# Optimization experiments

Hardware: AMD Instinct MI355X
Metric: run time of the kernel (lower is better)

Reference implementation:

```python
import jax, jax.numpy as jnp
import numpy as np

B, T, F, H, L = 16384, 24, 7, 8, 4
DENSE = [T * H, 1024, 2048, 4]


def setup_inputs() -> dict:
    key = jax.random.key(0)
    d = {"x": jax.random.normal(jax.random.fold_in(key, 0), (B, T, F), jnp.float32)}
    k = 1
    s = 1.0 / np.sqrt(H)  # torch LSTM init bound
    for l in range(L):
        in_dim = F if l == 0 else H
        for name, shape in [("Wih", (4 * H, in_dim)), ("Whh", (4 * H, H)), ("bih", (4 * H,)), ("bhh", (4 * H,))]:
            d[f"{name}{l}"] = jax.random.uniform(jax.random.fold_in(key, k), shape, jnp.float32, -s, s)
            k += 1
    for i in range(1, len(DENSE)):
        si = 1.0 / np.sqrt(DENSE[i - 1])
        d[f"Wd{i}"] = jax.random.uniform(jax.random.fold_in(key, k), (DENSE[i], DENSE[i - 1]), jnp.float32, -si, si)
        k += 1
        d[f"bd{i}"] = jax.random.uniform(jax.random.fold_in(key, k), (DENSE[i],), jnp.float32, -si, si)
        k += 1
    return d


def _lstm_layer(xs, Wih, Whh, b):
    # xs: [T, B, in] -> ys: [T, B, H]; torch gate order i,f,g,o
    Hn = Whh.shape[1]
    h0 = jnp.zeros((xs.shape[1], Hn), xs.dtype)

    def step(carry, xt):
        h, c = carry
        z = xt @ Wih.T + h @ Whh.T + b  # [B, 4H]
        i, f, g, o = jnp.split(z, 4, axis=-1)
        c = jax.nn.sigmoid(f) * c + jax.nn.sigmoid(i) * jnp.tanh(g)
        h = jax.nn.sigmoid(o) * jnp.tanh(c)
        return (h, c), h

    (_, _), ys = jax.lax.scan(step, (h0, h0), xs)
    return ys


def _forward(x, lstm_params, dense_params):
    xs = jnp.transpose(x, (1, 0, 2))  # [T, B, F]
    for (Wih, Whh, bih, bhh) in lstm_params:
        xs = _lstm_layer(xs, Wih, Whh, bih + bhh)
    out = jnp.transpose(xs, (1, 0, 2)).reshape(x.shape[0], T * H)  # [B, 192]
    (W1, b1), (W2, b2), (W3, b3) = dense_params
    out = jax.nn.relu(out @ W1.T + b1)
    out = jax.nn.relu(out @ W2.T + b2)
    return out @ W3.T + b3  # [B, num_classes]


def reference(x, Wih0, Whh0, bih0, bhh0, Wih1, Whh1, bih1, bhh1, Wih2, Whh2, bih2, bhh2, Wih3, Whh3, bih3, bhh3, Wd1, bd1, Wd2, bd2, Wd3, bd3):
    lstm_params = [(Wih0, Whh0, bih0, bhh0), (Wih1, Whh1, bih1, bhh1), (Wih2, Whh2, bih2, bhh2), (Wih3, Whh3, bih3, bhh3)]
    dense_params = [(Wd1, bd1), (Wd2, bd2), (Wd3, bd3)]
    return _forward(x, lstm_params, dense_params)
```

## Files before the change

kernel.cpp:

```cpp
#include <hip/hip_runtime.h>
#include <hip/hip_bf16.h>

typedef __attribute__((ext_vector_type(4))) float f32x4;
typedef __attribute__((ext_vector_type(16))) float f32x16;
typedef __attribute__((ext_vector_type(2))) float f32x2;
typedef __attribute__((ext_vector_type(8))) short bf16x8;

__device__ __forceinline__ ushort f2bf(float f) {
    union { float f; uint u; } v; v.f = f;
    uint u = v.u;
    return (ushort)((u + 0x7fffu + ((u >> 16) & 1u)) >> 16);
}
__device__ __forceinline__ float sigm(float x) {
    return __builtin_amdgcn_rcpf(1.0f + __builtin_amdgcn_exp2f(x * -1.442695040888963f));
}
__device__ __forceinline__ float tanh_(float x) {
    return 2.0f * __builtin_amdgcn_rcpf(1.0f + __builtin_amdgcn_exp2f(x * -2.885390081777927f)) - 1.0f;
}

typedef const __attribute__((address_space(1))) unsigned int ga_u32;
typedef __attribute__((address_space(3))) unsigned int lds_u32;
__device__ __forceinline__ void g2l16(const void* g, void* l) {
    __builtin_amdgcn_global_load_lds((ga_u32*)(unsigned long long)g,
                                     (lds_u32*)(unsigned int)(unsigned long long)l,
                                     16, 0, 0);
}

struct LstmW {
    const float* wih[4];
    const float* whh[4];
    const float* bih[4];
    const float* bhh[4];
};

__device__ __forceinline__ void gates8p(const f32x2 w01[8], const f32x2 w23[8],
                                        const float xv8[8], f32x2& a01, f32x2& a23) {
#pragma unroll
    for (int k = 0; k < 8; ++k) {
        f32x2 xv = {xv8[k], xv8[k]};
        a01 += w01[k] * xv;
        a23 += w23[k] * xv;
    }
}
__device__ __forceinline__ void cellup(f32x2 a01, f32x2 a23, float& h, float& c) {
    c = sigm(a01.y) * c + sigm(a01.x) * tanh_(a23.x);
    h = sigm(a23.y) * tanh_(c);
}
__device__ __forceinline__ void ld8(const float* p, float v[8]) {
    float4 a = *(const float4*)p;
    float4 b = *(const float4*)(p + 4);
    v[0] = a.x; v[1] = a.y; v[2] = a.z; v[3] = a.w;
    v[4] = b.x; v[5] = b.y; v[6] = b.z; v[7] = b.w;
}

__global__ __launch_bounds__(256) void pre_kernel(const float* __restrict__ x, LstmW p,
                                                  ushort* __restrict__ Y,
                                                  const float* __restrict__ W1,
                                                  const float* __restrict__ W2,
                                                  ushort* __restrict__ W1b,
                                                  ushort* __restrict__ W2b,
                                                  const float* __restrict__ b3,
                                                  float* __restrict__ out) {
    __shared__ float xs[32 * 168];
    __shared__ float hb[32 * 200];

    const int tid = threadIdx.x;
    if (blockIdx.x >= 512) {
        const int tg = (blockIdx.x - 512) * 256 + tid;
        if (tg < 16384) {
            float4 bv = {b3[0], b3[1], b3[2], b3[3]};
            ((float4*)out)[tg] = bv;
        }
#pragma unroll
        for (int s = 0; s < 4; ++s) {
            int i = tg + s * 143360;
            const float4* src; ushort4* dst; int off;
            if (i < 49152) { src = (const float4*)W1; dst = (ushort4*)W1b; off = i; }
            else { src = (const float4*)W2; dst = (ushort4*)W2b; off = i - 49152; }
            float4 v = src[off];
            ushort4 r; r.x = f2bf(v.x); r.y = f2bf(v.y); r.z = f2bf(v.z); r.w = f2bf(v.w);
            dst[off] = r;
        }
        return;
    }

    const int e0 = blockIdx.x * 32;
    {
        const float4* s = (const float4*)(x + (size_t)e0 * 168);
        float4* d = (float4*)xs;
        for (int i = tid; i < 1344; i += 256) d[i] = s[i];
    }
    __syncthreads();

    const int el = tid >> 3, j = tid & 7;
    float* hr = hb + el * 200;
    const float* xr = xs + el * 168;

    f32x2 wx01[8], wx23[8], wh01[8], wh23[8], b01, b23;

    {
        const float* Wih = p.wih[0];
        const float* Whh = p.whh[0];
#pragma unroll
        for (int k = 0; k < 7; ++k) {
            wx01[k] = {Wih[(0 + j) * 7 + k], Wih[(8 + j) * 7 + k]};
            wx23[k] = {Wih[(16 + j) * 7 + k], Wih[(24 + j) * 7 + k]};
        }
#pragma unroll
        for (int k = 0; k < 8; ++k) {
            wh01[k] = {Whh[(0 + j) * 8 + k], Whh[(8 + j) * 8 + k]};
            wh23[k] = {Whh[(16 + j) * 8 + k], Whh[(24 + j) * 8 + k]};
        }
        b01 = {p.bih[0][j] + p.bhh[0][j], p.bih[0][8 + j] + p.bhh[0][8 + j]};
        b23 = {p.bih[0][16 + j] + p.bhh[0][16 + j], p.bih[0][24 + j] + p.bhh[0][24 + j]};

        float h = 0.f, c = 0.f;
        {
            f32x2 a01 = b01, a23 = b23;
#pragma unroll
            for (int k = 0; k < 7; ++k) {
                f32x2 xv = {xr[k], xr[k]};
                a01 += wx01[k] * xv; a23 += wx23[k] * xv;
            }
            cellup(a01, a23, h, c);
            hr[j] = h;
        }
        for (int t = 1; t < 24; ++t) {
            f32x2 a01 = b01, a23 = b23;
#pragma unroll
            for (int k = 0; k < 7; ++k) {
                f32x2 xv = {xr[t * 7 + k], xr[t * 7 + k]};
                a01 += wx01[k] * xv; a23 += wx23[k] * xv;
            }
            float hp[8]; ld8(&hr[(t - 1) * 8], hp);
            gates8p(wh01, wh23, hp, a01, a23);
            cellup(a01, a23, h, c);
            hr[t * 8 + j] = h;
        }
    }

#pragma unroll
    for (int l = 1; l < 4; ++l) {
        const float* Wih = p.wih[l];
        const float* Whh = p.whh[l];
#pragma unroll
        for (int k = 0; k < 8; ++k) {
            wx01[k] = {Wih[(0 + j) * 8 + k], Wih[(8 + j) * 8 + k]};
            wx23[k] = {Wih[(16 + j) * 8 + k], Wih[(24 + j) * 8 + k]};
            wh01[k] = {Whh[(0 + j) * 8 + k], Whh[(8 + j) * 8 + k]};
            wh23[k] = {Whh[(16 + j) * 8 + k], Whh[(24 + j) * 8 + k]};
        }
        b01 = {p.bih[l][j] + p.bhh[l][j], p.bih[l][8 + j] + p.bhh[l][8 + j]};
        b23 = {p.bih[l][16 + j] + p.bhh[l][16 + j], p.bih[l][24 + j] + p.bhh[l][24 + j]};

        float h = 0.f, c = 0.f;
        {
            float xin[8]; ld8(&hr[0], xin);
            f32x2 a01 = b01, a23 = b23;
            gates8p(wx01, wx23, xin, a01, a23);
            cellup(a01, a23, h, c);
            hr[j] = h;
            if (l == 3) Y[((size_t)(e0 + el) * 24) * 8 + j] = f2bf(h);
        }
        for (int t = 1; t < 24; ++t) {
            float xin[8]; ld8(&hr[t * 8], xin);
            float hp[8];  ld8(&hr[(t - 1) * 8], hp);
            f32x2 a01 = b01, a23 = b23;
            gates8p(wx01, wx23, xin, a01, a23);
            gates8p(wh01, wh23, hp, a01, a23);
            cellup(a01, a23, h, c);
            hr[t * 8 + j] = h;
            if (l == 3) Y[((size_t)(e0 + el) * 24 + t) * 8 + j] = f2bf(h);
        }
    }
}

template <int KDIM>
__device__ __forceinline__ void gemm_body(const ushort* __restrict__ A,
                                          const ushort* __restrict__ W,
                                          const float* __restrict__ bias,
                                          ushort* __restrict__ Hout, int N) {
    __shared__ alignas(16) ushort smem[16384];
    ushort* As = smem;
    ushort* Ws = smem + 8192;

    const int tid = threadIdx.x;
    const int m0 = blockIdx.x * 128;
    const int n0 = blockIdx.y * 128;
    const int lane = tid & 63;
    const int wv = tid >> 6;
    const int wm = (wv & 1) * 64;
    const int wn = (wv >> 1) * 64;
    const int l31 = lane & 31;
    const int kh = lane >> 5;

    const int lrow = lane >> 3;
    const int lchunk = (lane & 7) ^ lrow;
    const ushort* Ag = A + (size_t)(m0 + wv * 32 + lrow) * KDIM + lchunk * 8;
    const ushort* Wg = W + (size_t)(n0 + wv * 32 + lrow) * KDIM + lchunk * 8;
    ushort* Ald = As + wv * 2048;
    ushort* Wld = Ws + wv * 2048;

    const int r7 = l31 & 7;
    const int arow0 = (wm + l31) * 64;
    const int brow0 = (wn + l31) * 64;

    f32x16 acc[2][2];
#pragma unroll
    for (int mi = 0; mi < 2; ++mi)
#pragma unroll
        for (int ni = 0; ni < 2; ++ni)
#pragma unroll
            for (int r = 0; r < 16; ++r) acc[mi][ni][r] = 0.f;

    for (int k0 = 0; k0 < KDIM; k0 += 64) {
#pragma unroll
        for (int c = 0; c < 4; ++c)
            g2l16(Ag + (size_t)c * 8 * KDIM + k0, Ald + c * 512);
#pragma unroll
        for (int c = 0; c < 4; ++c)
            g2l16(Wg + (size_t)c * 8 * KDIM + k0, Wld + c * 512);
        __syncthreads();

#pragma unroll
        for (int ks = 0; ks < 4; ++ks) {
            const int ck = ((ks * 2 + kh) ^ r7) * 8;
            bf16x8 afr[2], bfr[2];
#pragma unroll
            for (int mi = 0; mi < 2; ++mi)
                afr[mi] = *(const bf16x8*)&As[arow0 + mi * 2048 + ck];
#pragma unroll
            for (int ni = 0; ni < 2; ++ni)
                bfr[ni] = *(const bf16x8*)&Ws[brow0 + ni * 2048 + ck];
#pragma unroll
            for (int mi = 0; mi < 2; ++mi)
#pragma unroll
                for (int ni = 0; ni < 2; ++ni)
                    acc[mi][ni] = __builtin_amdgcn_mfma_f32_32x32x16_bf16(afr[mi], bfr[ni],
                                                                         acc[mi][ni], 0, 0, 0);
        }
        __syncthreads();
    }

#pragma unroll
    for (int ni = 0; ni < 2; ++ni) {
        const int col = n0 + wn + ni * 32 + l31;
        const float b = bias[col];
#pragma unroll
        for (int mi = 0; mi < 2; ++mi)
#pragma unroll
            for (int r = 0; r < 16; ++r) {
                const int row = m0 + wm + mi * 32 + (r & 3) + 8 * (r >> 2) + 4 * kh;
                Hout[(size_t)row * N + col] = f2bf(fmaxf(acc[mi][ni][r] + b, 0.f));
            }
    }
}

__global__ __launch_bounds__(256, 4) void gemm1_kernel(const ushort* __restrict__ A,
                                                       const ushort* __restrict__ W,
                                                       const float* __restrict__ bias,
                                                       ushort* __restrict__ Hout, int N) {
    gemm_body<192>(A, W, bias, Hout, N);
}

template <int OFFB>
__device__ __forceinline__ bf16x8 dsr(unsigned a) {
    bf16x8 r;
    asm volatile("ds_read_b128 %0, %1 offset:%2"
                 : "=v"(r) : "v"(a), "i"(OFFB));
    return r;
}
template <int B>
__device__ __forceinline__ void ld_ah_asm(unsigned p0, unsigned p1, bf16x8 fr[8]) {
    fr[0] = dsr<B + 0>(p0);    fr[1] = dsr<B + 0>(p1);
    fr[2] = dsr<B + 2048>(p0); fr[3] = dsr<B + 2048>(p1);
    fr[4] = dsr<B + 4096>(p0); fr[5] = dsr<B + 4096>(p1);
    fr[6] = dsr<B + 6144>(p0); fr[7] = dsr<B + 6144>(p1);
}
template <int B>
__device__ __forceinline__ void ld_bh_asm(unsigned p0, unsigned p1, bf16x8 fr[4]) {
    fr[0] = dsr<B + 0>(p0);    fr[1] = dsr<B + 0>(p1);
    fr[2] = dsr<B + 2048>(p0); fr[3] = dsr<B + 2048>(p1);
}
template <int QA, int QB>
__device__ __forceinline__ void mma_quad(f32x4 acc[8][4], const bf16x8 afr[8],
                                         const bf16x8 bfr[4]) {
#pragma unroll
    for (int ks = 0; ks < 2; ++ks)
#pragma unroll
        for (int mi = 0; mi < 4; ++mi)
#pragma unroll
            for (int ni = 0; ni < 2; ++ni)
                acc[QA * 4 + mi][QB * 2 + ni] = __builtin_amdgcn_mfma_f32_16x16x32_bf16(
                    afr[mi * 2 + ks], bfr[ni * 2 + ks], acc[QA * 4 + mi][QB * 2 + ni],
                    0, 0, 0);
}

#define SBAR() __builtin_amdgcn_s_barrier()
#define MMA_GATE() do { SBAR(); \
    asm volatile("s_waitcnt lgkmcnt(0)"); \
    __builtin_amdgcn_sched_barrier(0); } while (0)
#define CLUSTER_END() do { __builtin_amdgcn_s_setprio(0); \
    __builtin_amdgcn_sched_barrier(0); } while (0)

__global__ __launch_bounds__(512) void gemm2_kernel(const ushort* __restrict__ A,
                                                    const ushort* __restrict__ W,
                                                    const float* __restrict__ bias,
                                                    const float* __restrict__ W3,
                                                    float* __restrict__ outf) {
    __shared__ alignas(16) ushort smem[65536];
    __shared__ alignas(16) float w3s[1040];

    const int tid = threadIdx.x;
    const int wg = ((int)blockIdx.x & 7) * 64 + ((int)blockIdx.x >> 3);
    const int m0 = (wg >> 3) << 8;
    const int n0 = (wg & 7) << 8;

    const int lane = tid & 63;
    const int wv = tid >> 6;

    const int lrow = tid >> 3;
    const int lc8 = ((tid & 7) ^ (lrow & 7)) << 3;
    const ushort* Ag = A + (size_t)(m0 + lrow) * 1024 + lc8;
    const ushort* Bg = W + (size_t)(n0 + lrow) * 1024 + lc8;
    ushort* const sA0 = smem;
    ushort* const sB0 = smem + 16384;
    ushort* const sA1 = smem + 32768;
    ushort* const sB1 = smem + 49152;
    const int srow64 = (wv << 3) * 64;

    const int l15 = lane & 15, kq = lane >> 4, r7 = l15 & 7;
    const int wM = wv >> 2, wN = wv & 3;
    const unsigned sbase = (unsigned)(unsigned long long)&smem[0];
    const unsigned pc0B = (unsigned)((kq ^ r7) << 4);
    const unsigned pc1B = pc0B ^ 64u;
    const unsigned aRowB = (unsigned)((wM * 128 + l15) * 128);
    const unsigned bRowB = (unsigned)((wN * 64 + l15) * 128);
    const unsigned aA0p0 = sbase + aRowB + pc0B;
    const unsigned aA0p1 = sbase + aRowB + pc1B;
    const unsigned aA1p0 = aA0p0 + 65536u;
    const unsigned aA1p1 = aA0p1 + 65536u;
    const unsigned bB0p0 = sbase + 32768u + bRowB + pc0B;
    const unsigned bB0p1 = sbase + 32768u + bRowB + pc1B;
    const unsigned bB1p0 = bB0p0 + 65536u;
    const unsigned bB1p1 = bB0p1 + 65536u;

    auto stA = [&](int buf, int h, int kt) {
        ushort* b = buf ? sA1 : sA0;
#pragma unroll
        for (int c = 0; c < 2; ++c)
            g2l16(Ag + (size_t)(h * 128 + c * 64) * 1024 + kt * 64,
                  b + (h * 128 + c * 64) * 64 + srow64);
    };
    auto stB = [&](int buf, int h, int kt) {
        ushort* b = buf ? sB1 : sB0;
#pragma unroll
        for (int c = 0; c < 2; ++c)
            g2l16(Bg + (size_t)(h * 128 + c * 64) * 1024 + kt * 64,
                  b + (h * 128 + c * 64) * 64 + srow64);
    };

    f32x4 acc[8][4];
#pragma unroll
    for (int i = 0; i < 8; ++i)
#pragma unroll
        for (int j = 0; j < 4; ++j)
#pragma unroll
            for (int r = 0; r < 4; ++r) acc[i][j][r] = 0.f;

#pragma unroll
    for (int i = 0; i < 2; ++i) {
        int idx = tid + i * 512;
        w3s[(idx >> 8) * 260 + (idx & 255)] = W3[(size_t)(idx >> 8) * 2048 + n0 + (idx & 255)];
    }
    float bias4[4];
#pragma unroll
    for (int ni = 0; ni < 4; ++ni) bias4[ni] = bias[n0 + wN * 64 + ni * 16 + l15];

    stA(0, 0, 0); stB(0, 0, 0); stB(0, 1, 0); stA(0, 1, 0);
    stB(1, 0, 1); stB(1, 1, 1);
    asm volatile("s_waitcnt vmcnt(0)" ::: "memory");
    SBAR();

    bf16x8 afr[8], b0r[4], b1r[4];
#pragma unroll 1
    for (int it = 0; it < 8; ++it) {
        const int k1 = 2 * it + 1, k2 = 2 * it + 2, k3 = 2 * it + 3;
        const bool nl = (it < 7);
        ld_ah_asm<0>(aA0p0, aA0p1, afr);
        ld_bh_asm<0>(bB0p0, bB0p1, b0r);
        stA(1, 0, k1);
        MMA_GATE();
        __builtin_amdgcn_s_setprio(1);
        mma_quad<0, 0>(acc, afr, b0r);
        CLUSTER_END();
        SBAR();
        ld_bh_asm<4096>(bB0p0, bB0p1, b1r);
        stA(1, 1, k1);
        MMA_GATE();
        __builtin_amdgcn_s_setprio(1);
        mma_quad<0, 1>(acc, afr, b1r);
        CLUSTER_END();
        SBAR();
        ld_ah_asm<8192>(aA0p0, aA0p1, afr);
        if (nl) stB(0, 0, k2);
        MMA_GATE();
        __builtin_amdgcn_s_setprio(1);
        mma_quad<1, 1>(acc, afr, b1r);
        CLUSTER_END();
        SBAR();
        if (nl) stB(0, 1, k2);
        MMA_GATE();
        __builtin_amdgcn_s_setprio(1);
        mma_quad<1, 0>(acc, afr, b0r);
        CLUSTER_END();
        if (nl) { asm volatile("s_waitcnt vmcnt(4)" ::: "memory"); }
        else    { asm volatile("s_waitcnt vmcnt(0)" ::: "memory"); }
        SBAR();
        ld_ah_asm<8192>(aA1p0, aA1p1, afr);
        ld_bh_asm<0>(bB1p0, bB1p1, b0r);
        if (nl) stA(0, 0, k2);
        MMA_GATE();
        __builtin_amdgcn_s_setprio(1);
        mma_quad<1, 0>(acc, afr, b0r);
        CLUSTER_END();
        SBAR();
        ld_bh_asm<4096>(bB1p0, bB1p1, b1r);
        if (nl) stA(0, 1, k2);
        MMA_GATE();
        __builtin_amdgcn_s_setprio(1);
        mma_quad<1, 1>(acc, afr, b1r);
        CLUSTER_END();
        SBAR();
        ld_ah_asm<0>(aA1p0, aA1p1, afr);
        if (nl) stB(1, 0, k3);
        MMA_GATE();
        __builtin_amdgcn_s_setprio(1);
        mma_quad<0, 1>(acc, afr, b1r);
        CLUSTER_END();
        SBAR();
        if (nl) stB(1, 1, k3);
        MMA_GATE();
        __builtin_amdgcn_s_setprio(1);
        mma_quad<0, 0>(acc, afr, b0r);
        CLUSTER_END();
        if (nl) { asm volatile("s_waitcnt vmcnt(4)" ::: "memory"); }
        SBAR();
    }

    float* Cs = (float*)smem;
    const int drow = tid >> 3;
    const int cls = (tid & 7) >> 1;
    const int hf = tid & 1;
    const float* wrow = &w3s[cls * 260 + hf * 128];
    __syncthreads();
#pragma unroll
    for (int s = 0; s < 4; ++s) {
        if (wM == (s >> 1)) {
            const int mb = (s & 1) * 4;
#pragma unroll
            for (int mi = 0; mi < 4; ++mi)
#pragma unroll
                for (int ni = 0; ni < 4; ++ni) {
                    f32x4 v = acc[mb + mi][ni];
                    const int cbase = (mi * 16 + kq * 4) * 260 + wN * 64 + ni * 16 + l15;
#pragma unroll
                    for (int r = 0; r < 4; ++r)
                        Cs[cbase + r * 260] = fmaxf(v[r] + bias4[ni], 0.f);
                }
        }
        __syncthreads();
        {
            const float* crow = &Cs[drow * 260 + hf * 128];
            float p = 0.f;
#pragma unroll
            for (int ch = 0; ch < 64; ++ch) {
                f32x2 cv = *(const f32x2*)(crow + ch * 2);
                f32x2 wv2 = *(const f32x2*)(wrow + ch * 2);
                p += cv.x * wv2.x + cv.y * wv2.y;
            }
            p += __shfl_xor(p, 1);
            if (hf == 0)
                atomicAdd(&outf[(size_t)(m0 + s * 64 + drow) * 4 + cls], p);
        }
        __syncthreads();
    }
}

extern "C" void kernel_launch(void* const* d_in, const int* in_sizes, int n_in,
                              void* d_out, int out_size, void* d_ws, size_t ws_size,
                              hipStream_t stream) {
    const float* x = (const float*)d_in[0];
    LstmW w;
    for (int l = 0; l < 4; ++l) {
        w.wih[l] = (const float*)d_in[1 + 4 * l];
        w.whh[l] = (const float*)d_in[2 + 4 * l];
        w.bih[l] = (const float*)d_in[3 + 4 * l];
        w.bhh[l] = (const float*)d_in[4 + 4 * l];
    }
    const float* Wd1 = (const float*)d_in[17];
    const float* bd1 = (const float*)d_in[18];
    const float* Wd2 = (const float*)d_in[19];
    const float* bd2 = (const float*)d_in[20];
    const float* Wd3 = (const float*)d_in[21];
    const float* bd3 = (const float*)d_in[22];
    float* out = (float*)d_out;

    ushort* Y   = (ushort*)d_ws;
    ushort* H1  = (ushort*)((char*)d_ws + 6291456);
    ushort* W1b = (ushort*)((char*)d_ws + 39845888);
    ushort* W2b = (ushort*)((char*)d_ws + 40239104);

    pre_kernel<<<1072, 256, 0, stream>>>(x, w, Y, Wd1, Wd2, W1b, W2b, bd3, out);
    gemm1_kernel<<<dim3(128, 8), 256, 0, stream>>>(Y, W1b, bd1, H1, 1024);
    gemm2_kernel<<<512, 512, 0, stream>>>(H1, W2b, bd2, Wd3, out);
}
```

Baseline: 223.3 us.

## Split MFMA quads by k-step and interleave LDS fragment loads with partial lgkmcnt waits

Restructures the gemm2 main loop so each MFMA quad is split into two k-sub-steps, with LDS fragment reads for the next sub-step issued between them and gated by partial lgkmcnt waits instead of a full wait. Half of each fragment set is preloaded before the barrier, and the first fragments are prefetched before the loop and at the end of each iteration. The vmcnt thresholds are tightened to match the reordered global-to-LDS stores. This aims to hide LDS read latency behind MFMA execution, but the hand-tuned wait counts and barrier placement make races or stalls easy to introduce.

```diff
diff --git a/kernel.cpp b/kernel.cpp
--- a/kernel.cpp
+++ b/kernel.cpp
@@ -270,38 +270,24 @@
                  : "=v"(r) : "v"(a), "i"(OFFB));
     return r;
 }
-template <int B>
-__device__ __forceinline__ void ld_ah_asm(unsigned p0, unsigned p1, bf16x8 fr[8]) {
-    fr[0] = dsr<B + 0>(p0);    fr[1] = dsr<B + 0>(p1);
-    fr[2] = dsr<B + 2048>(p0); fr[3] = dsr<B + 2048>(p1);
-    fr[4] = dsr<B + 4096>(p0); fr[5] = dsr<B + 4096>(p1);
-    fr[6] = dsr<B + 6144>(p0); fr[7] = dsr<B + 6144>(p1);
-}
-template <int B>
-__device__ __forceinline__ void ld_bh_asm(unsigned p0, unsigned p1, bf16x8 fr[4]) {
-    fr[0] = dsr<B + 0>(p0);    fr[1] = dsr<B + 0>(p1);
-    fr[2] = dsr<B + 2048>(p0); fr[3] = dsr<B + 2048>(p1);
-}
-template <int QA, int QB>
-__device__ __forceinline__ void mma_quad(f32x4 acc[8][4], const bf16x8 afr[8],
-                                         const bf16x8 bfr[4]) {
-#pragma unroll
-    for (int ks = 0; ks < 2; ++ks)
-#pragma unroll
-        for (int mi = 0; mi < 4; ++mi)
-#pragma unroll
-            for (int ni = 0; ni < 2; ++ni)
-                acc[QA * 4 + mi][QB * 2 + ni] = __builtin_amdgcn_mfma_f32_16x16x32_bf16(
-                    afr[mi * 2 + ks], bfr[ni * 2 + ks], acc[QA * 4 + mi][QB * 2 + ni],
-                    0, 0, 0);
-}
-
-#define SBAR() __builtin_amdgcn_s_barrier()
-#define MMA_GATE() do { SBAR(); \
-    asm volatile("s_waitcnt lgkmcnt(0)"); \
-    __builtin_amdgcn_sched_barrier(0); } while (0)
-#define CLUSTER_END() do { __builtin_amdgcn_s_setprio(0); \
-    __builtin_amdgcn_sched_barrier(0); } while (0)
+template <int QA, int QB, int KS>
+__device__ __forceinline__ void mma_sub(f32x4 acc[8][4], const bf16x8 afr[8],
+                                        const bf16x8 br[4]) {
+#pragma unroll
+    for (int mi = 0; mi < 4; ++mi)
+#pragma unroll
+        for (int ni = 0; ni < 2; ++ni)
+            acc[QA * 4 + mi][QB * 2 + ni] = __builtin_amdgcn_mfma_f32_16x16x32_bf16(
+                afr[mi * 2 + KS], br[ni * 2 + KS], acc[QA * 4 + mi][QB * 2 + ni],
+                0, 0, 0);
+}
+
+#define SBAR()  __builtin_amdgcn_s_barrier()
+#define SCHED0() __builtin_amdgcn_sched_barrier(0)
+#define LGKM(N) do { asm volatile("s_waitcnt lgkmcnt(" #N ")"); SCHED0(); } while (0)
+#define VMC(N)  do { asm volatile("s_waitcnt vmcnt(" #N ")" ::: "memory"); } while (0)
+#define PRIO1() __builtin_amdgcn_s_setprio(1)
+#define PRIO0() do { __builtin_amdgcn_s_setprio(0); SCHED0(); } while (0)
 
 __global__ __launch_bounds__(512) void gemm2_kernel(const ushort* __restrict__ A,
                                                     const ushort* __restrict__ W,
@@ -377,75 +363,81 @@
 #pragma unroll
     for (int ni = 0; ni < 4; ++ni) bias4[ni] = bias[n0 + wN * 64 + ni * 16 + l15];
 
-    stA(0, 0, 0); stB(0, 0, 0); stB(0, 1, 0); stA(0, 1, 0);
+    stA(0, 0, 0); stA(0, 1, 0); stB(0, 0, 0); stB(0, 1, 0);
     stB(1, 0, 1); stB(1, 1, 1);
-    asm volatile("s_waitcnt vmcnt(0)" ::: "memory");
-    SBAR();
+    asm volatile("s_waitcnt lgkmcnt(0)");
+    VMC(4);
+    SBAR(); SCHED0();
 
     bf16x8 afr[8], b0r[4], b1r[4];
+    afr[0] = dsr<0>(aA0p0);    afr[2] = dsr<2048>(aA0p0);
+    afr[4] = dsr<4096>(aA0p0); afr[6] = dsr<6144>(aA0p0);
+    b0r[0] = dsr<0>(bB0p0);    b0r[2] = dsr<2048>(bB0p0);
+
 #pragma unroll 1
     for (int it = 0; it < 8; ++it) {
         const int k1 = 2 * it + 1, k2 = 2 * it + 2, k3 = 2 * it + 3;
         const bool nl = (it < 7);
-        ld_ah_asm<0>(aA0p0, aA0p1, afr);
-        ld_bh_asm<0>(bB0p0, bB0p1, b0r);
+        SBAR(); SCHED0();
+        afr[1] = dsr<0>(aA0p1);    afr[3] = dsr<2048>(aA0p1);
+        afr[5] = dsr<4096>(aA0p1); afr[7] = dsr<6144>(aA0p1);
+        b0r[1] = dsr<0>(bB0p1);    b0r[3] = dsr<2048>(bB0p1);
         stA(1, 0, k1);
-        MMA_GATE();
-        __builtin_amdgcn_s_setprio(1);
-        mma_quad<0, 0>(acc, afr, b0r);
-        CLUSTER_END();
-        SBAR();
-        ld_bh_asm<4096>(bB0p0, bB0p1, b1r);
+        LGKM(6); PRIO1(); mma_sub<0, 0, 0>(acc, afr, b0r); PRIO0();
+        b1r[0] = dsr<4096>(bB0p0); b1r[2] = dsr<6144>(bB0p0);
+        LGKM(2); PRIO1(); mma_sub<0, 0, 1>(acc, afr, b0r); PRIO0();
+        SBAR(); SCHED0();
+        b1r[1] = dsr<4096>(bB0p1); b1r[3] = dsr<6144>(bB0p1);
         stA(1, 1, k1);
-        MMA_GATE();
-        __builtin_amdgcn_s_setprio(1);
-        mma_quad<0, 1>(acc, afr, b1r);
-        CLUSTER_END();
-        SBAR();
-        ld_ah_asm<8192>(aA0p0, aA0p1, afr);
+        LGKM(2); PRIO1(); mma_sub<0, 1, 0>(acc, afr, b1r); PRIO0();
+        afr[0] = dsr<8192>(aA0p0);  afr[2] = dsr<10240>(aA0p0);
+        afr[4] = dsr<12288>(aA0p0); afr[6] = dsr<14336>(aA0p0);
+        LGKM(4); PRIO1(); mma_sub<0, 1, 1>(acc, afr, b1r); PRIO0();
+        SBAR(); SCHED0();
+        afr[1] = dsr<8192>(aA0p1);  afr[3] = dsr<10240>(aA0p1);
+        afr[5] = dsr<12288>(aA0p1); afr[7] = dsr<14336>(aA0p1);
         if (nl) stB(0, 0, k2);
-        MMA_GATE();
-        __builtin_amdgcn_s_setprio(1);
-        mma_quad<1, 1>(acc, afr, b1r);
-        CLUSTER_END();
-        SBAR();
+        LGKM(4); PRIO1(); mma_sub<1, 1, 0>(acc, afr, b1r); PRIO0();
+        LGKM(0); PRIO1(); mma_sub<1, 1, 1>(acc, afr, b1r); PRIO0();
+        if (nl) { VMC(2); } else { VMC(0); }
+        SBAR(); SCHED0();
         if (nl) stB(0, 1, k2);
-        MMA_GATE();
-        __builtin_amdgcn_s_setprio(1);
-        mma_quad<1, 0>(acc, afr, b0r);
-        CLUSTER_END();
-        if (nl) { asm volatile("s_waitcnt vmcnt(4)" ::: "memory"); }
-        else    { asm volatile("s_waitcnt vmcnt(0)" ::: "memory"); }
-        SBAR();
-        ld_ah_asm<8192>(aA1p0, aA1p1, afr);
-        ld_bh_asm<0>(bB1p0, bB1p1, b0r);
+        PRIO1(); mma_sub<1, 0, 0>(acc, afr, b0r); PRIO0();
+        afr[0] = dsr<8192>(aA1p0);  afr[2] = dsr<10240>(aA1p0);
+        afr[4] = dsr<12288>(aA1p0); afr[6] = dsr<14336>(aA1p0);
+        b0r[0] = dsr<0>(bB1p0);     b0r[2] = dsr<2048>(bB1p0);
+        PRIO1(); mma_sub<1, 0, 1>(acc, afr, b0r); PRIO0();
+        SBAR(); SCHED0();
+        afr[1] = dsr<8192>(aA1p1);  afr[3] = dsr<10240>(aA1p1);
+        afr[5] = dsr<12288>(aA1p1); afr[7] = dsr<14336>(aA1p1);
+        b0r[1] = dsr<0>(bB1p1);     b0r[3] = dsr<2048>(bB1p1);
         if (nl) stA(0, 0, k2);
-        MMA_GATE();
-        __builtin_amdgcn_s_setprio(1);
-        mma_quad<1, 0>(acc, afr, b0r);
-        CLUSTER_END();
-        SBAR();
-        ld_bh_asm<4096>(bB1p0, bB1p1, b1r);
+        LGKM(6); PRIO1(); mma_sub<1, 0, 0>(acc, afr, b0r); PRIO0();
+        b1r[0] = dsr<4096>(bB1p0); b1r[2] = dsr<6144>(bB1p0);
+        LGKM(2); PRIO1(); mma_sub<1, 0, 1>(acc, afr, b0r); PRIO0();
+        SBAR(); SCHED0();
+        b1r[1] = dsr<4096>(bB1p1); b1r[3] = dsr<6144>(bB1p1);
         if (nl) stA(0, 1, k2);
-        MMA_GATE();
-        __builtin_amdgcn_s_setprio(1);
-        mma_quad<1, 1>(acc, afr, b1r);
-        CLUSTER_END();
-        SBAR();
-        ld_ah_asm<0>(aA1p0, aA1p1, afr);
+        LGKM(2); PRIO1(); mma_sub<1, 1, 0>(acc, afr, b1r); PRIO0();
+        afr[0] = dsr<0>(aA1p0);    afr[2] = dsr<2048>(aA1p0);
+        afr[4] = dsr<4096>(aA1p0); afr[6] = dsr<6144>(aA1p0);
+        LGKM(4); PRIO1(); mma_sub<1, 1, 1>(acc, afr, b1r); PRIO0();
+        SBAR(); SCHED0();
+        afr[1] = dsr<0>(aA1p1);    afr[3] = dsr<2048>(aA1p1);
+        afr[5] = dsr<4096>(aA1p1); afr[7] = dsr<6144>(aA1p1);
         if (nl) stB(1, 0, k3);
-        MMA_GATE();
-        __builtin_amdgcn_s_setprio(1);
-        mma_quad<0, 1>(acc, afr, b1r);
-        CLUSTER_END();
-        SBAR();
+        LGKM(4); PRIO1(); mma_sub<0, 1, 0>(acc, afr, b1r); PRIO0();
+        LGKM(0); PRIO1(); mma_sub<0, 1, 1>(acc, afr, b1r); PRIO0();
+        VMC(2);
+        SBAR(); SCHED0();
         if (nl) stB(1, 1, k3);
-        MMA_GATE();
-        __builtin_amdgcn_s_setprio(1);
-        mma_quad<0, 0>(acc, afr, b0r);
-        CLUSTER_END();
-        if (nl) { asm volatile("s_waitcnt vmcnt(4)" ::: "memory"); }
-        SBAR();
+        PRIO1(); mma_sub<0, 0, 0>(acc, afr, b0r); PRIO0();
+        if (nl) {
+            afr[0] = dsr<0>(aA0p0);    afr[2] = dsr<2048>(aA0p0);
+            afr[4] = dsr<4096>(aA0p0); afr[6] = dsr<6144>(aA0p0);
+            b0r[0] = dsr<0>(bB0p0);    b0r[2] = dsr<2048>(bB0p0);
+        }
+        PRIO1(); mma_sub<0, 0, 1>(acc, afr, b0r); PRIO0();
     }
 
     float* Cs = (float*)smem;
```

New measurement: 210.0 us. 1.06x faster.
